# Performance work log

Hardware: AMD Instinct MI355X
Metric: run time of the kernel (lower is better)

## Reference

```python
import jax, jax.numpy as jnp
import numpy as np

PATCH = 9  # patch_size (kernel_size=1, stride=1, padding=0, dilation_patch=1)


def setup_inputs() -> dict:
    key = jax.random.key(0)
    k1, k2 = jax.random.split(key)
    B, C, H, W = 4, 256, 128, 128
    return {
        "input1": jax.random.normal(k1, (B, C, H, W), dtype=jnp.float32),
        "input2": jax.random.normal(k2, (B, C, H, W), dtype=jnp.float32),
    }


def _correlation(input1, input2, patch=PATCH):
    # Faithful to torch _correlation_patch_based fast path:
    # corr[b, dy*P+dx, h, w] = sum_c input1[b,c,h,w] * input2_pad[b,c,h+dy,w+dx]
    # where input2 is zero-padded by P//2 (matches F.unfold padding=P//2).
    B, C, H, W = input1.shape
    pad = patch // 2
    i2p = jnp.pad(input2, ((0, 0), (0, 0), (pad, pad), (pad, pad)))
    # displacement offsets in unfold order: ky-major, kx-minor
    offs = jnp.stack(
        jnp.meshgrid(jnp.arange(patch), jnp.arange(patch), indexing="ij"), axis=-1
    ).reshape(-1, 2)  # (P*P, 2)

    def body(carry, off):
        # shifted window of input2, same (B,C,H,W) footprint (no unfold blowup)
        win = jax.lax.dynamic_slice(i2p, (0, 0, off[0], off[1]), (B, C, H, W))
        return carry, jnp.einsum("bchw,bchw->bhw", input1, win)

    _, corr = jax.lax.scan(body, None, offs)  # (P*P, B, H, W)
    return jnp.transpose(corr, (1, 0, 2, 3))  # (B, P*P, H, W)


def reference(input1, input2):
    return _correlation(input1, input2)
```

## Files before the change

kernel.cpp:

```cpp
#include <hip/hip_runtime.h>

#define BB   4
#define CC   256
#define HH   128
#define WW   128
#define PAD  4
#define KOUT 81

#define TH   8
#define SW   16
#define KC   32
#define NCHUNK (CC / KC)
#define AK   40

typedef _Float16 half8 __attribute__((ext_vector_type(8)));
typedef float    f32x4 __attribute__((ext_vector_type(4)));

__global__ __launch_bounds__(512, 4)
void corr_mfma2(const float* __restrict__ i1,
                const float* __restrict__ i2,
                float* __restrict__ out)
{
    __shared__ _Float16 Ald[128 * AK];
    __shared__ _Float16 Bld[512 * AK];

    const int t    = threadIdx.x;
    const int wave = t >> 6;
    const int lane = t & 63;
    const int l15  = lane & 15;
    const int quad = lane >> 4;

    const int b  = blockIdx.z;
    const int h0 = blockIdx.y * TH;
    const int w0 = blockIdx.x * SW;

    const size_t strideC = (size_t)HH * WW;
    const float* i1b = i1 + (size_t)b * CC * strideC;
    const float* i2b = i2 + (size_t)b * CC * strideC;

    bool valid;
    const float* gptr;
    _Float16* ldst;
    if (t < 384) {
        const int sq  = t % 24;
        const int sr  = t / 24;
        const int col = w0 - PAD + sq;
        const int row = h0 - PAD + sr;
        valid = (col >= 0) && (col < WW) && (row >= 0) && (row < HH);
        const int crow = valid ? row : 0;
        const int ccol = valid ? col : 0;
        gptr = i2b + (size_t)crow * WW + ccol;
        ldst = &Bld[(sr * 32 + sq) * AK];
    } else {
        const int i  = t - 384;
        const int sm = i & 15;
        const int sr = i >> 4;
        valid = true;
        gptr = i1b + (size_t)(h0 + sr) * WW + (w0 + sm);
        ldst = &Ald[(sr * 16 + sm) * AK];
    }

    f32x4 acc[9][2];
#pragma unroll
    for (int dy = 0; dy < 9; ++dy) {
        acc[dy][0] = (f32x4){0.f, 0.f, 0.f, 0.f};
        acc[dy][1] = (f32x4){0.f, 0.f, 0.f, 0.f};
    }

    float v[KC];

#pragma unroll
    for (int j = 0; j < KC; ++j)
        v[j] = valid ? gptr[(size_t)j * strideC] : 0.f;
#pragma unroll
    for (int u = 0; u < 4; ++u) {
        half8 hv;
#pragma unroll
        for (int k = 0; k < 8; ++k) hv[k] = (_Float16)v[8 * u + k];
        *(half8*)&ldst[8 * u] = hv;
    }
    __syncthreads();

#pragma unroll 1
    for (int ch = 0; ch < NCHUNK; ++ch) {
        if (ch + 1 < NCHUNK) {
            const float* g = gptr + (size_t)(ch + 1) * KC * strideC;
#pragma unroll
            for (int j = 0; j < KC; ++j)
                v[j] = valid ? g[(size_t)j * strideC] : 0.f;
        }

        {
            const half8 a = *(const half8*)&Ald[(wave * 16 + l15) * AK + quad * 8];
#pragma unroll
            for (int dy = 0; dy < 9; ++dy) {
                const int r = wave + dy;
                const half8 b0 = *(const half8*)&Bld[(r * 32 + l15) * AK + quad * 8];
                acc[dy][0] = __builtin_amdgcn_mfma_f32_16x16x32_f16(a, b0, acc[dy][0], 0, 0, 0);
                const half8 b1 = *(const half8*)&Bld[(r * 32 + 16 + l15) * AK + quad * 8];
                acc[dy][1] = __builtin_amdgcn_mfma_f32_16x16x32_f16(a, b1, acc[dy][1], 0, 0, 0);
            }
        }

        if (ch + 1 < NCHUNK) {
            __syncthreads();
#pragma unroll
            for (int u = 0; u < 4; ++u) {
                half8 hv;
#pragma unroll
                for (int k = 0; k < 8; ++k) hv[k] = (_Float16)v[8 * u + k];
                *(half8*)&ldst[8 * u] = hv;
            }
            __syncthreads();
        }
    }

    const int h = h0 + wave;
#pragma unroll
    for (int dy = 0; dy < 9; ++dy) {
#pragma unroll
        for (int tt = 0; tt < 2; ++tt) {
#pragma unroll
            for (int reg = 0; reg < 4; ++reg) {
                const int p  = quad * 4 + reg;
                const int dx = l15 + 16 * tt - p;
                if (dx >= 0 && dx <= 8) {
                    out[(((size_t)b * KOUT + (dy * 9 + dx)) * HH + h) * WW + (w0 + p)] =
                        acc[dy][tt][reg];
                }
            }
        }
    }
}

extern "C" void kernel_launch(void* const* d_in, const int* in_sizes, int n_in,
                              void* d_out, int out_size, void* d_ws, size_t ws_size,
                              hipStream_t stream)
{
    (void)in_sizes; (void)n_in; (void)d_ws; (void)ws_size; (void)out_size;
    const float* i1 = (const float*)d_in[0];
    const float* i2 = (const float*)d_in[1];
    float* out = (float*)d_out;

    dim3 grid(WW / SW, HH / TH, BB);
    dim3 block(512);
    corr_mfma2<<<grid, block, 0, stream>>>(i1, i2, out);
}
```

Measured before the change: 186.2 us.

## Split dy displacements across three block groups to raise occupancy and parallelism

```diff
diff --git a/kernel.cpp b/kernel.cpp
--- a/kernel.cpp
+++ b/kernel.cpp
@@ -7,22 +7,25 @@
 #define PAD  4
 #define KOUT 81
 
-#define TH   8
-#define SW   16
-#define KC   32
+#define TH    8
+#define SW    16
+#define KC    32
 #define NCHUNK (CC / KC)
-#define AK   40
+#define NG    3
+#define BROWS 11
+#define BPTS  (BROWS * 24)
+#define APTS  (TH * 16)
+#define AK    40
 
 typedef _Float16 half8 __attribute__((ext_vector_type(8)));
 typedef float    f32x4 __attribute__((ext_vector_type(4)));
 
-__global__ __launch_bounds__(512, 4)
-void corr_mfma2(const float* __restrict__ i1,
+__global__ __launch_bounds__(512, 6)
+void corr_mfma3(const float* __restrict__ i1,
                 const float* __restrict__ i2,
                 float* __restrict__ out)
 {
-    __shared__ _Float16 Ald[128 * AK];
-    __shared__ _Float16 Bld[512 * AK];
+    __shared__ _Float16 sh[(BPTS + APTS) * AK];
 
     const int t    = threadIdx.x;
     const int wave = t >> 6;
@@ -30,7 +33,9 @@
     const int l15  = lane & 15;
     const int quad = lane >> 4;
 
-    const int b  = blockIdx.z;
+    const int z  = blockIdx.z;
+    const int b  = z / NG;
+    const int g  = z - b * NG;
     const int h0 = blockIdx.y * TH;
     const int w0 = blockIdx.x * SW;
 
@@ -38,72 +43,43 @@
     const float* i1b = i1 + (size_t)b * CC * strideC;
     const float* i2b = i2 + (size_t)b * CC * strideC;
 
-    bool valid;
-    const float* gptr;
-    _Float16* ldst;
-    if (t < 384) {
+    const bool stager = (t < BPTS + APTS);
+    bool valid = false;
+    const float* gptr = i1b;
+    _Float16* ldst = sh;
+    if (t < BPTS) {
         const int sq  = t % 24;
         const int sr  = t / 24;
         const int col = w0 - PAD + sq;
-        const int row = h0 - PAD + sr;
+        const int row = h0 - PAD + 3 * g + sr;
         valid = (col >= 0) && (col < WW) && (row >= 0) && (row < HH);
-        const int crow = valid ? row : 0;
-        const int ccol = valid ? col : 0;
-        gptr = i2b + (size_t)crow * WW + ccol;
-        ldst = &Bld[(sr * 32 + sq) * AK];
-    } else {
-        const int i  = t - 384;
+        gptr  = i2b + (size_t)(valid ? row : 0) * WW + (valid ? col : 0);
+        ldst  = &sh[(sr * 24 + sq) * AK];
+    } else if (stager) {
+        const int i  = t - BPTS;
         const int sm = i & 15;
         const int sr = i >> 4;
         valid = true;
-        gptr = i1b + (size_t)(h0 + sr) * WW + (w0 + sm);
-        ldst = &Ald[(sr * 16 + sm) * AK];
+        gptr  = i1b + (size_t)(h0 + sr) * WW + (w0 + sm);
+        ldst  = &sh[(BPTS + sr * 16 + sm) * AK];
     }
 
-    f32x4 acc[9][2];
+    f32x4 acc[NG][2];
 #pragma unroll
-    for (int dy = 0; dy < 9; ++dy) {
-        acc[dy][0] = (f32x4){0.f, 0.f, 0.f, 0.f};
-        acc[dy][1] = (f32x4){0.f, 0.f, 0.f, 0.f};
+    for (int dd = 0; dd < NG; ++dd) {
+        acc[dd][0] = (f32x4){0.f, 0.f, 0.f, 0.f};
+        acc[dd][1] = (f32x4){0.f, 0.f, 0.f, 0.f};
     }
-
-    float v[KC];
-
-#pragma unroll
-    for (int j = 0; j < KC; ++j)
-        v[j] = valid ? gptr[(size_t)j * strideC] : 0.f;
-#pragma unroll
-    for (int u = 0; u < 4; ++u) {
-        half8 hv;
-#pragma unroll
-        for (int k = 0; k < 8; ++k) hv[k] = (_Float16)v[8 * u + k];
-        *(half8*)&ldst[8 * u] = hv;
-    }
-    __syncthreads();
 
 #pragma unroll 1
     for (int ch = 0; ch < NCHUNK; ++ch) {
-        if (ch + 1 < NCHUNK) {
-            const float* g = gptr + (size_t)(ch + 1) * KC * strideC;
+        if (ch > 0) __syncthreads();
+        if (stager) {
+            const float* gp = gptr + (size_t)ch * KC * strideC;
+            float v[KC];
 #pragma unroll
             for (int j = 0; j < KC; ++j)
-                v[j] = valid ? g[(size_t)j * strideC] : 0.f;
-        }
-
-        {
-            const half8 a = *(const half8*)&Ald[(wave * 16 + l15) * AK + quad * 8];
-#pragma unroll
-            for (int dy = 0; dy < 9; ++dy) {
-                const int r = wave + dy;
-                const half8 b0 = *(const half8*)&Bld[(r * 32 + l15) * AK + quad * 8];
-                acc[dy][0] = __builtin_amdgcn_mfma_f32_16x16x32_f16(a, b0, acc[dy][0], 0, 0, 0);
-                const half8 b1 = *(const half8*)&Bld[(r * 32 + 16 + l15) * AK + quad * 8];
-                acc[dy][1] = __builtin_amdgcn_mfma_f32_16x16x32_f16(a, b1, acc[dy][1], 0, 0, 0);
-            }
-        }
-
-        if (ch + 1 < NCHUNK) {
-            __syncthreads();
+                v[j] = valid ? gp[(size_t)j * strideC] : 0.f;
 #pragma unroll
             for (int u = 0; u < 4; ++u) {
                 half8 hv;
@@ -111,13 +87,24 @@
                 for (int k = 0; k < 8; ++k) hv[k] = (_Float16)v[8 * u + k];
                 *(half8*)&ldst[8 * u] = hv;
             }
-            __syncthreads();
+        }
+        __syncthreads();
+
+        const half8 a = *(const half8*)&sh[(BPTS + wave * 16 + l15) * AK + quad * 8];
+#pragma unroll
+        for (int dd = 0; dd < NG; ++dd) {
+            const int r = wave + dd;
+            const half8 b0 = *(const half8*)&sh[(r * 24 + l15) * AK + quad * 8];
+            acc[dd][0] = __builtin_amdgcn_mfma_f32_16x16x32_f16(a, b0, acc[dd][0], 0, 0, 0);
+            const half8 b1 = *(const half8*)&sh[(r * 24 + 16 + l15) * AK + quad * 8];
+            acc[dd][1] = __builtin_amdgcn_mfma_f32_16x16x32_f16(a, b1, acc[dd][1], 0, 0, 0);
         }
     }
 
     const int h = h0 + wave;
 #pragma unroll
-    for (int dy = 0; dy < 9; ++dy) {
+    for (int dd = 0; dd < NG; ++dd) {
+        const int dy = 3 * g + dd;
 #pragma unroll
         for (int tt = 0; tt < 2; ++tt) {
 #pragma unroll
@@ -126,7 +113,7 @@
                 const int dx = l15 + 16 * tt - p;
                 if (dx >= 0 && dx <= 8) {
                     out[(((size_t)b * KOUT + (dy * 9 + dx)) * HH + h) * WW + (w0 + p)] =
-                        acc[dy][tt][reg];
+                        acc[dd][tt][reg];
                 }
             }
         }
@@ -142,7 +129,7 @@
     const float* i2 = (const float*)d_in[1];
     float* out = (float*)d_out;
 
-    dim3 grid(WW / SW, HH / TH, BB);
+    dim3 grid(WW / SW, HH / TH, BB * NG);
     dim3 block(512);
-    corr_mfma2<<<grid, block, 0, stream>>>(i1, i2, out);
+    corr_mfma3<<<grid, block, 0, stream>>>(i1, i2, out);
 }
```

New measurement: 363.2 us. 1.95x slower.
